# Optimization experiments

Measured on AMD Instinct MI355X. Metric: run time of the kernel, lower is better.

## Reference

```python
import jax, jax.numpy as jnp
import numpy as np

SCALE_EXP = 1.0
DIM = 64      # per-head dim
HEADS = 16
C = 1.5 - SCALE_EXP  # = 0.5

B, L, D_IN = 4, 2048, 1024


def setup_inputs() -> dict:
    key = jax.random.key(0)
    k1, k2, k3 = jax.random.split(key, 3)
    x = jax.random.normal(k1, (B, L, D_IN), dtype=jnp.float32)
    # kernel_init for qk: normal(stddev = dim**(c-0.5)) = dim**0 = 1 for scale_exp=1
    Wqk = jax.random.normal(k2, (D_IN, 2 * HEADS * DIM), dtype=jnp.float32) * (DIM ** (C - 0.5))
    bqk = jnp.zeros((2 * HEADS * DIM,), dtype=jnp.float32)
    Wv = jax.random.normal(k3, (D_IN, HEADS * DIM), dtype=jnp.float32)  # stddev 1.0
    bv = jnp.zeros((HEADS * DIM,), dtype=jnp.float32)
    return {"x": x, "Wqk": Wqk, "bqk": bqk, "Wv": Wv, "bv": bv}


def reference(x, Wqk, bqk, Wv, bv):
    d_in = x.shape[-1]
    # qk projection, scaled by d_in**c
    qk = (x @ Wqk + bqk) / (d_in ** C)            # [b, l, 2*h*d]
    b, l, _ = qk.shape
    qk = qk.reshape(b, l, HEADS, 2 * DIM).transpose(0, 2, 1, 3)  # [b, h, l, 2d]
    q, k = jnp.split(qk, 2, axis=-1)              # each [b, h, l, d]
    v = (x @ Wv + bv) / jnp.sqrt(jnp.asarray(d_in, x.dtype))
    v = v.reshape(b, l, HEADS, DIM).transpose(0, 2, 1, 3)        # [b, h, l, d]
    A = (1.0 / (DIM ** SCALE_EXP)) * jnp.einsum('bhqd,bhkd->bhqk', q, k)
    phi_A = jax.nn.softmax(A, axis=-1)
    out = jnp.einsum('bhqk,bhkd->bhqd', phi_A, v)                # [b, h, l, d]
    return out.transpose(0, 2, 1, 3).reshape(b, l, HEADS * DIM)  # [b, l, h*d]
```

## Files before the change

kernel.cpp:

```cpp
#include <hip/hip_runtime.h>
#include <hip/hip_bf16.h>

typedef __attribute__((ext_vector_type(8))) short bf16x8;
typedef __attribute__((ext_vector_type(4))) float f32x4;
typedef __hip_bfloat16 bf16;

#define MFMA_16x16x32(a, b, c) __builtin_amdgcn_mfma_f32_16x16x32_bf16((a), (b), (c), 0, 0, 0)

#define ASM_VMCNT2()  asm volatile("s_waitcnt vmcnt(2)" ::: "memory")
#define ASM_VMCNT0()  asm volatile("s_waitcnt vmcnt(0)" ::: "memory")
#define ASM_BARRIER() asm volatile("s_waitcnt lgkmcnt(0)\n\ts_barrier" ::: "memory")

typedef __attribute__((address_space(1))) void as1_void;
typedef __attribute__((address_space(3))) void as3_void;

__device__ __forceinline__ void g2lds16(const void* g, void* l) {
  __builtin_amdgcn_global_load_lds((as1_void*)(void*)g, (as3_void*)l, 16, 0, 0);
}

__global__ __launch_bounds__(256) void prep(const float* __restrict__ x, bf16* __restrict__ xb,
                                            const float* __restrict__ Wqk,
                                            const float* __restrict__ Wv,
                                            bf16* __restrict__ Wt) {
  __shared__ float tile[32][33];
  const int bid = blockIdx.x, tid = threadIdx.x;
  if (bid < 4096) {
    const float scale = 1.f / 32.f;
    int i = bid * 256 + tid;
    const float4* s4 = (const float4*)x;
    float4 f0 = s4[i * 2], f1 = s4[i * 2 + 1];
    float vals[8] = {f0.x, f0.y, f0.z, f0.w, f1.x, f1.y, f1.z, f1.w};
    union { unsigned short u[8]; uint4 v; } o;
#pragma unroll
    for (int j = 0; j < 8; ++j) {
      bf16 hv = __float2bfloat16(vals[j] * scale);
      o.u[j] = *(unsigned short*)&hv;
    }
    ((uint4*)xb)[i] = o.v;
    return;
  }
  const float* src;
  bf16* dst;
  int N, n0, k0;
  if (bid < 6144) {
    int t = bid - 4096;
    src = Wqk; dst = Wt; N = 2048;
    n0 = (t & 63) * 32; k0 = (t >> 6) * 32;
  } else {
    int t = bid - 6144;
    src = Wv; dst = Wt + (size_t)2048 * 1024; N = 1024;
    n0 = (t & 31) * 32; k0 = (t >> 5) * 32;
  }
  const int tx = tid & 31, ty = tid >> 5;
#pragma unroll
  for (int i = 0; i < 4; ++i) {
    int kl = i * 8 + ty;
    tile[kl][tx] = src[(size_t)(k0 + kl) * N + n0 + tx];
  }
  __syncthreads();
#pragma unroll
  for (int i = 0; i < 4; ++i) {
    int nl = i * 8 + ty;
    dst[(size_t)(n0 + nl) * 1024 + k0 + tx] = __float2bfloat16(tile[tx][nl]);
  }
}

__global__ __launch_bounds__(256) void proj_gemm(
    const bf16* __restrict__ A, const bf16* __restrict__ Bt,
    const float* __restrict__ bqk, const float* __restrict__ bv,
    bf16* __restrict__ Qb, bf16* __restrict__ Kb, bf16* __restrict__ Vtb) {
  __shared__ __align__(16) bf16 As[128 * 32];
  __shared__ __align__(16) bf16 Bs[128 * 32];
  const int tid = threadIdx.x, lane = tid & 63, w = tid >> 6;
  const int wm = w >> 1, wn = w & 1;
  const int l15 = lane & 15, g = lane >> 4;
  const int m0 = blockIdx.x * 128, n0 = blockIdx.y * 128;

  f32x4 acc[4][4];
#pragma unroll
  for (int i = 0; i < 4; ++i)
#pragma unroll
    for (int j = 0; j < 4; ++j) acc[i][j] = (f32x4)0.f;

  const bf16* ap[2];
  const bf16* bp[2];
  unsigned off[2];
#pragma unroll
  for (int i = 0; i < 2; ++i) {
    int s = i * 256 + tid;
    int row = s >> 2, pos = s & 3;
    int kp = ((pos ^ ((row >> 1) & 3)) << 3);
    ap[i] = A + (size_t)(m0 + row) * 1024 + kp;
    bp[i] = Bt + (size_t)(n0 + row) * 1024 + kp;
    off[i] = (i * 256 + w * 64) * 8;
  }

  const int swc = (l15 >> 1) & 3;

  for (int kt = 0; kt < 32; ++kt) {
    if (kt) ASM_BARRIER();
#pragma unroll
    for (int i = 0; i < 2; ++i) {
      g2lds16(ap[i], &As[off[i]]);
      g2lds16(bp[i], &Bs[off[i]]);
      ap[i] += 32;
      bp[i] += 32;
    }
    ASM_VMCNT0();
    ASM_BARRIER();

    bf16x8 af[4], bfr[4];
#pragma unroll
    for (int f = 0; f < 4; ++f) {
      af[f]  = *(const bf16x8*)&As[(wm * 64 + f * 16 + l15) * 32 + ((g ^ swc) << 3)];
      bfr[f] = *(const bf16x8*)&Bs[(wn * 64 + f * 16 + l15) * 32 + ((g ^ swc) << 3)];
    }
#pragma unroll
    for (int fm = 0; fm < 4; ++fm)
#pragma unroll
      for (int fn = 0; fn < 4; ++fn)
        acc[fm][fn] = MFMA_16x16x32(af[fm], bfr[fn], acc[fm][fn]);
  }

  const float INV32 = 1.f / 32.f;
  const float QSCALE = 0.125f * 1.44269504088896340736f;
#pragma unroll
  for (int fm = 0; fm < 4; ++fm) {
#pragma unroll
    for (int fn = 0; fn < 4; ++fn) {
      int n = n0 + wn * 64 + fn * 16 + l15;
#pragma unroll
      for (int r = 0; r < 4; ++r) {
        int m = m0 + wm * 64 + fm * 16 + 4 * g + r;
        int b = m >> 11, lrow = m & 2047;
        float val = acc[fm][fn][r];
        if (n < 2048) {
          float vb = val + bqk[n] * INV32;
          int h = n >> 7, wi = n & 127;
          if (wi < 64) Qb[(((size_t)b * 16 + h) * 2048 + lrow) * 64 + wi] = __float2bfloat16(vb * QSCALE);
          else         Kb[(((size_t)b * 16 + h) * 2048 + lrow) * 64 + (wi - 64)] = __float2bfloat16(vb * 0.125f);
        } else {
          int nv = n - 2048;
          val = val + bv[nv] * INV32;
          int h = nv >> 6, d = nv & 63;
          Vtb[(((size_t)b * 16 + h) * 64 + d) * 2048 + lrow] = __float2bfloat16(val);
        }
      }
    }
  }
}

__global__ __launch_bounds__(512) void attn(
    const bf16* __restrict__ Qb, const bf16* __restrict__ Kb,
    const bf16* __restrict__ Vtb, float* __restrict__ out) {
  __shared__ __align__(16) bf16 Ks[2][64 * 64];
  __shared__ __align__(16) bf16 Vs[2][64 * 64];

  const int bh = blockIdx.x;
  const int qt = blockIdx.y;
  const int b = bh >> 4, h = bh & 15;
  const int tid = threadIdx.x, lane = tid & 63, w = tid >> 6;
  const int l15 = lane & 15, g = lane >> 4;

  const bf16* Kbh = Kb + (size_t)bh * 2048 * 64;
  const bf16* Vbh = Vtb + (size_t)bh * 64 * 2048;

  const bf16* qbase = Qb + ((size_t)bh * 2048 + qt * 128 + w * 16) * 64;
  bf16x8 qa[2];
#pragma unroll
  for (int ks = 0; ks < 2; ++ks)
    qa[ks] = *(const bf16x8*)(qbase + (size_t)l15 * 64 + ks * 32 + g * 8);

  bf16x8 aone;
#pragma unroll
  for (int j = 0; j < 8; ++j) aone[j] = (l15 == 0) ? (short)0x3F80 : (short)0;

  f32x4 acc[5];
#pragma unroll
  for (int da = 0; da < 5; ++da) acc[da] = (f32x4)0.f;

  const bf16* kp;
  const bf16* vp;
  unsigned ldsoff;
  {
    int s = tid;
    int row = s >> 3, blk = s & 7;
    int swk = (row & 3) | ((row & 8) >> 1);
    kp = Kbh + (size_t)row * 64 + ((blk ^ swk) << 3);
    vp = Vbh + (size_t)row * 2048 + ((blk ^ (row & 7)) << 3);
    ldsoff = (unsigned)s * 8;
  }

  auto stage = [&](int bufi) {
    g2lds16(kp, &Ks[bufi][ldsoff]);
    g2lds16(vp, &Vs[bufi][ldsoff]);
    kp += 64 * 64;
    vp += 64;
  };

  stage(0);
  int cur = 0;
  const f32x4 z4 = (f32x4)0.f;

  for (int t = 0; t < 32; ++t) {
    if (t < 31) { stage(cur ^ 1); ASM_VMCNT2(); }
    else        { ASM_VMCNT0(); }
    ASM_BARRIER();

    f32x4 s_acc[4];
    __builtin_amdgcn_s_setprio(1);
#pragma unroll
    for (int kb = 0; kb < 4; ++kb) {
      const int krow = ((kb & 2) << 4) + ((l15 >> 2) << 3) + ((kb & 1) << 2) + (l15 & 3);
      const int swk = (krow & 3) | ((krow & 8) >> 1);
      bf16x8 ak0 = *(const bf16x8*)&Ks[cur][krow * 64 + ((g ^ swk) << 3)];
      bf16x8 ak1 = *(const bf16x8*)&Ks[cur][krow * 64 + (((4 + g) ^ swk) << 3)];
      s_acc[kb] = MFMA_16x16x32(ak1, qa[1], MFMA_16x16x32(ak0, qa[0], z4));
    }
    __builtin_amdgcn_s_setprio(0);

    bf16x8 pb[2];
#pragma unroll
    for (int ks = 0; ks < 2; ++ks) {
      union { unsigned int u[4]; bf16x8 v; } pk;
#pragma unroll
      for (int u = 0; u < 4; ++u) {
        const int kbp = 2 * ks + (u >> 1);
        const int r0 = (2 * u) & 3;
        float lo = __builtin_amdgcn_exp2f(s_acc[kbp][r0]);
        float hi = __builtin_amdgcn_exp2f(s_acc[kbp][r0 + 1]);
        __hip_bfloat162 h2 = __float22bfloat162_rn(float2{lo, hi});
        pk.u[u] = *(unsigned int*)&h2;
      }
      pb[ks] = pk.v;
    }

    __builtin_amdgcn_s_setprio(1);
#pragma unroll
    for (int ks = 0; ks < 2; ++ks) {
#pragma unroll
      for (int da = 0; da < 4; ++da) {
        const int vrow = da * 16 + l15;
        bf16x8 av = *(const bf16x8*)&Vs[cur][vrow * 64 + (((ks * 4 + g) ^ (l15 & 7)) << 3)];
        acc[da] = MFMA_16x16x32(av, pb[ks], acc[da]);
      }
      acc[4] = MFMA_16x16x32(aone, pb[ks], acc[4]);
    }
    __builtin_amdgcn_s_setprio(0);

    if (t < 31) ASM_BARRIER();
    cur ^= 1;
  }

  {
    const float lsum = __shfl(acc[4][0], l15, 64);
    const float inv = 1.f / lsum;
    const int lrow = qt * 128 + w * 16 + l15;
    float* orow = out + ((size_t)b * 2048 + lrow) * 1024 + h * 64 + 4 * g;
#pragma unroll
    for (int da = 0; da < 4; ++da) {
      float4 o4 = {acc[da][0] * inv, acc[da][1] * inv,
                   acc[da][2] * inv, acc[da][3] * inv};
      *(float4*)(orow + da * 16) = o4;
    }
  }
}

extern "C" void kernel_launch(void* const* d_in, const int* in_sizes, int n_in,
                              void* d_out, int out_size, void* d_ws, size_t ws_size,
                              hipStream_t stream) {
  (void)in_sizes; (void)n_in; (void)out_size; (void)ws_size;
  const float* x   = (const float*)d_in[0];
  const float* Wqk = (const float*)d_in[1];
  const float* bqk = (const float*)d_in[2];
  const float* Wv  = (const float*)d_in[3];
  const float* bv  = (const float*)d_in[4];
  float* outp = (float*)d_out;

  char* ws = (char*)d_ws;
  bf16* xb  = (bf16*)(ws);
  bf16* Wt  = (bf16*)(ws + 16777216);
  bf16* Qb  = (bf16*)(ws + 23068672);
  bf16* Kb  = (bf16*)(ws + 39845888);
  bf16* Vtb = (bf16*)(ws + 56623104);

  prep<<<7168, 256, 0, stream>>>(x, xb, Wqk, Wv, Wt);
  proj_gemm<<<dim3(64, 24), 256, 0, stream>>>(xb, Wt, bqk, bv, Qb, Kb, Vtb);
  attn<<<dim3(64, 16), 512, 0, stream>>>(Qb, Kb, Vtb, outp);
}
```

Measured before the change: 186.4 us.

## Triple-buffer projection GEMM with larger 128x256 tiles and BK=64

The projection GEMM now uses 512 threads with a 128x256 output tile and a K-step of 64. Tiles are staged through a three-deep LDS ring with asynchronous global-to-LDS loads issued two stages ahead, and an XOR swizzle avoids bank conflicts. The goal is to hide global load latency behind MFMA work, where the old kernel waited for each tile to arrive, and to improve operand reuse. In exchange it uses much more LDS (about 144KB), which lowers occupancy, and halves the grid to 768 blocks.

```diff
diff --git a/kernel.cpp b/kernel.cpp
--- a/kernel.cpp
+++ b/kernel.cpp
@@ -7,6 +7,7 @@
 
 #define MFMA_16x16x32(a, b, c) __builtin_amdgcn_mfma_f32_16x16x32_bf16((a), (b), (c), 0, 0, 0)
 
+#define ASM_VMCNT6()  asm volatile("s_waitcnt vmcnt(6)" ::: "memory")
 #define ASM_VMCNT2()  asm volatile("s_waitcnt vmcnt(2)" ::: "memory")
 #define ASM_VMCNT0()  asm volatile("s_waitcnt vmcnt(0)" ::: "memory")
 #define ASM_BARRIER() asm volatile("s_waitcnt lgkmcnt(0)\n\ts_barrier" ::: "memory")
@@ -65,16 +66,17 @@
   }
 }
 
-__global__ __launch_bounds__(256) void proj_gemm(
+__global__ __launch_bounds__(512) void proj_gemm(
     const bf16* __restrict__ A, const bf16* __restrict__ Bt,
     const float* __restrict__ bqk, const float* __restrict__ bv,
     bf16* __restrict__ Qb, bf16* __restrict__ Kb, bf16* __restrict__ Vtb) {
-  __shared__ __align__(16) bf16 As[128 * 32];
-  __shared__ __align__(16) bf16 Bs[128 * 32];
+  __shared__ __align__(16) bf16 As[3][128 * 64];
+  __shared__ __align__(16) bf16 Bs[3][256 * 64];
   const int tid = threadIdx.x, lane = tid & 63, w = tid >> 6;
-  const int wm = w >> 1, wn = w & 1;
+  const int wm = w >> 2, wn = w & 3;
   const int l15 = lane & 15, g = lane >> 4;
-  const int m0 = blockIdx.x * 128, n0 = blockIdx.y * 128;
+  const int m0 = blockIdx.x * 128, n0 = blockIdx.y * 256;
+  const int swz = l15 & 7;
 
   f32x4 acc[4][4];
 #pragma unroll
@@ -83,43 +85,58 @@
     for (int j = 0; j < 4; ++j) acc[i][j] = (f32x4)0.f;
 
   const bf16* ap[2];
-  const bf16* bp[2];
-  unsigned off[2];
+  unsigned offA[2];
 #pragma unroll
   for (int i = 0; i < 2; ++i) {
-    int s = i * 256 + tid;
-    int row = s >> 2, pos = s & 3;
-    int kp = ((pos ^ ((row >> 1) & 3)) << 3);
-    ap[i] = A + (size_t)(m0 + row) * 1024 + kp;
-    bp[i] = Bt + (size_t)(n0 + row) * 1024 + kp;
-    off[i] = (i * 256 + w * 64) * 8;
-  }
-
-  const int swc = (l15 >> 1) & 3;
-
-  for (int kt = 0; kt < 32; ++kt) {
-    if (kt) ASM_BARRIER();
-#pragma unroll
-    for (int i = 0; i < 2; ++i) {
-      g2lds16(ap[i], &As[off[i]]);
-      g2lds16(bp[i], &Bs[off[i]]);
-      ap[i] += 32;
-      bp[i] += 32;
-    }
-    ASM_VMCNT0();
+    int s = i * 512 + tid, r = s >> 3, c = s & 7;
+    ap[i] = A + (size_t)(m0 + r) * 1024 + ((c ^ (r & 7)) << 3);
+    offA[i] = (unsigned)s * 8;
+  }
+  const bf16* bp[4];
+  unsigned offB[4];
+#pragma unroll
+  for (int i = 0; i < 4; ++i) {
+    int s = i * 512 + tid, r = s >> 3, c = s & 7;
+    bp[i] = Bt + (size_t)(n0 + r) * 1024 + ((c ^ (r & 7)) << 3);
+    offB[i] = (unsigned)s * 8;
+  }
+
+  auto stage = [&](int bufi) {
+#pragma unroll
+    for (int i = 0; i < 2; ++i) { g2lds16(ap[i], &As[bufi][offA[i]]); ap[i] += 64; }
+#pragma unroll
+    for (int i = 0; i < 4; ++i) { g2lds16(bp[i], &Bs[bufi][offB[i]]); bp[i] += 64; }
+  };
+
+  stage(0);
+  stage(1);
+
+  for (int kt = 0; kt < 16; ++kt) {
+    if (kt < 15) ASM_VMCNT6();
+    else         ASM_VMCNT0();
     ASM_BARRIER();
-
-    bf16x8 af[4], bfr[4];
-#pragma unroll
-    for (int f = 0; f < 4; ++f) {
-      af[f]  = *(const bf16x8*)&As[(wm * 64 + f * 16 + l15) * 32 + ((g ^ swc) << 3)];
-      bfr[f] = *(const bf16x8*)&Bs[(wn * 64 + f * 16 + l15) * 32 + ((g ^ swc) << 3)];
-    }
-#pragma unroll
-    for (int fm = 0; fm < 4; ++fm)
-#pragma unroll
-      for (int fn = 0; fn < 4; ++fn)
-        acc[fm][fn] = MFMA_16x16x32(af[fm], bfr[fn], acc[fm][fn]);
+    if (kt + 2 < 16) stage((kt + 2) % 3);
+
+    const bf16* Ac = &As[kt % 3][0];
+    const bf16* Bc = &Bs[kt % 3][0];
+
+    bf16x8 af[2][4];
+#pragma unroll
+    for (int ks = 0; ks < 2; ++ks)
+#pragma unroll
+      for (int fm = 0; fm < 4; ++fm)
+        af[ks][fm] = *(const bf16x8*)&Ac[(wm * 64 + fm * 16 + l15) * 64 + (((ks * 4 + g) ^ swz) << 3)];
+
+    __builtin_amdgcn_s_setprio(1);
+#pragma unroll
+    for (int fn = 0; fn < 4; ++fn) {
+      bf16x8 bq0 = *(const bf16x8*)&Bc[(wn * 64 + fn * 16 + l15) * 64 + ((g ^ swz) << 3)];
+      bf16x8 bq1 = *(const bf16x8*)&Bc[(wn * 64 + fn * 16 + l15) * 64 + (((4 + g) ^ swz) << 3)];
+#pragma unroll
+      for (int fm = 0; fm < 4; ++fm)
+        acc[fm][fn] = MFMA_16x16x32(af[1][fm], bq1, MFMA_16x16x32(af[0][fm], bq0, acc[fm][fn]));
+    }
+    __builtin_amdgcn_s_setprio(0);
   }
 
   const float INV32 = 1.f / 32.f;
@@ -285,6 +302,6 @@
   bf16* Vtb = (bf16*)(ws + 56623104);
 
   prep<<<7168, 256, 0, stream>>>(x, xb, Wqk, Wv, Wt);
-  proj_gemm<<<dim3(64, 24), 256, 0, stream>>>(xb, Wt, bqk, bv, Qb, Kb, Vtb);
+  proj_gemm<<<dim3(64, 12), 512, 0, stream>>>(xb, Wt, bqk, bv, Qb, Kb, Vtb);
   attn<<<dim3(64, 16), 512, 0, stream>>>(Qb, Kb, Vtb, outp);
 }
```

Result: slower. 198.4 us (+6.4%).
